# Kernel tuning notes

Measured on AMD Instinct MI355X. Metric: run time of the kernel, lower is better.

## Reference

```python
import jax, jax.numpy as jnp
import numpy as np

GROUP = 128  # WNA16 quantization group size along input dim


def dequant_uint4(packed, scale, zp):
    """packed: [..., K//2] int32 holding two uint4 nibbles per element.
    scale, zp: [..., K//GROUP] float. Returns [..., K] float weights."""
    lo = jnp.bitwise_and(packed, 15)
    hi = jnp.bitwise_and(jnp.right_shift(packed, 4), 15)
    q = jnp.stack([lo, hi], axis=-1).reshape(*packed.shape[:-1], -1)  # [..., K]
    K = q.shape[-1]
    qg = q.astype(scale.dtype).reshape(*q.shape[:-1], K // GROUP, GROUP)
    w = (qg - zp[..., None]) * scale[..., None]
    return w.reshape(*q.shape)


def setup_inputs() -> dict:
    key = jax.random.key(0)
    ks = jax.random.split(key, 9)
    E, T, D, I = 8, 2048, 2048, 2816
    s13 = 1.0 / (8.0 * np.sqrt(D))   # keep dequantized weights ~unit-variance scale
    s2 = 1.0 / (8.0 * np.sqrt(I))
    x = jax.random.normal(ks[0], (T, D), jnp.float32)
    topk_ids = jax.random.randint(ks[1], (T, 2), 0, E, dtype=jnp.int32)
    tw = jax.random.uniform(ks[2], (T, 2), jnp.float32) + 0.1
    topk_weights = tw / tw.sum(-1, keepdims=True)
    w13_packed = jax.random.randint(ks[3], (E, 2 * I, D // 2), 0, 256, dtype=jnp.int32)
    w13_scale = (jax.random.uniform(ks[4], (E, 2 * I, D // GROUP), jnp.float32) + 0.5) * s13
    w13_zp = jax.random.uniform(ks[5], (E, 2 * I, D // GROUP), jnp.float32) * 16.0
    w2_packed = jax.random.randint(ks[6], (E, D, I // 2), 0, 256, dtype=jnp.int32)
    w2_scale = (jax.random.uniform(ks[7], (E, D, I // GROUP), jnp.float32) + 0.5) * s2
    w2_zp = jax.random.uniform(ks[8], (E, D, I // GROUP), jnp.float32) * 16.0
    return {"x": x, "topk_ids": topk_ids, "topk_weights": topk_weights,
            "w13_packed": w13_packed, "w13_scale": w13_scale, "w13_zp": w13_zp,
            "w2_packed": w2_packed, "w2_scale": w2_scale, "w2_zp": w2_zp}


def reference(x, topk_ids, topk_weights, w13_packed, w13_scale, w13_zp,
              w2_packed, w2_scale, w2_zp):
    E = w13_packed.shape[0]
    # Dequantize per-expert int4 weights (the get_dequant_weight loop)
    W13 = dequant_uint4(w13_packed, w13_scale, w13_zp)   # [E, 2I, D]
    W2 = dequant_uint4(w2_packed, w2_scale, w2_zp)       # [E, D, I]
    # mixture_of_experts with silu activation: gate/up proj, silu-mul, down proj
    gate_up = jnp.einsum('td,eid->tei', x, W13)           # [T, E, 2I]
    g, u = jnp.split(gate_up, 2, axis=-1)
    h = jax.nn.silu(g) * u                                # [T, E, I]
    y = jnp.einsum('tei,edi->ted', h, W2)                 # [T, E, D]
    # combine top-k routed experts with router weights
    route = jnp.einsum('tke,tk->te',
                       jax.nn.one_hot(topk_ids, E, dtype=x.dtype), topk_weights)
    out = jnp.einsum('ted,te->td', y, route)              # [T, D]
    return out
```

## Files before the change

### kernel.cpp

```cpp
#include <hip/hip_runtime.h>
#include <hip/hip_bf16.h>

#define T_TOK 2048
#define DDIM  2048
#define IDIM  2816
#define NE    8
#define NPAIR (T_TOK*2)
#define GU_N  (2*IDIM)

typedef __bf16  bf16x8 __attribute__((ext_vector_type(8)));
typedef float   f32x4  __attribute__((ext_vector_type(4)));
typedef int     int4v  __attribute__((ext_vector_type(4)));
typedef unsigned int uint4v __attribute__((ext_vector_type(4)));

#define OFF_A   (64*1024)
#define OFF_GU  (OFF_A  + (size_t)NPAIR*DDIM*2)
#define OFF_H   (OFF_GU + (size_t)NPAIR*GU_N*2)
#define OFF_YP  (OFF_H  + (size_t)NPAIR*IDIM*2)
#define W13_DWORDS (NE*(size_t)GU_N*(DDIM/8))
#define W2_DWORDS  (NE*(size_t)DDIM*(IDIM/8))

__device__ __forceinline__ unsigned short f2bf(float f) {
    __hip_bfloat16 h = __float2bfloat16(f);
    return __builtin_bit_cast(unsigned short, h);
}
__device__ __forceinline__ float bf2f(unsigned short u) {
    unsigned int x = ((unsigned int)u) << 16;
    return __builtin_bit_cast(float, x);
}
__device__ __forceinline__ unsigned int pack2bf(float lo, float hi) {
    return ((unsigned int)f2bf(hi) << 16) | (unsigned int)f2bf(lo);
}
__device__ __forceinline__ void gload_lds16(const void* g, void* l) {
    __builtin_amdgcn_global_load_lds(
        (const __attribute__((address_space(1))) void*)g,
        (__attribute__((address_space(3))) void*)l, 16, 0, 0);
}

__global__ void route_kernel(const int* __restrict__ ids, int* __restrict__ meta) {
    __shared__ int histL[NE][256];
    __shared__ int totals[NE];
    __shared__ int offsS[NE];
    const int tid = threadIdx.x;
    for (int e = 0; e < NE; ++e) histL[e][tid] = 0;
    for (int j = 0; j < 16; ++j) {
        int id = ids[tid*16 + j];
        histL[id][tid]++;
    }
    __syncthreads();
    if (tid < NE) {
        int run = 0;
        for (int i = 0; i < 256; ++i) { int v = histL[tid][i]; histL[tid][i] = run; run += v; }
        totals[tid] = run;
    }
    __syncthreads();
    if (tid == 0) {
        int run = 0;
        for (int e = 0; e < NE; ++e) {
            offsS[e] = run;
            meta[e] = totals[e];
            meta[8+e] = run;
            run += totals[e];
        }
    }
    __syncthreads();
    for (int j = 0; j < 16; ++j) {
        int p = tid*16 + j;
        int id = ids[p];
        int local = histL[id][tid];
        histL[id][tid] = local + 1;
        meta[64 + offsS[id] + local] = p;
    }
}

__global__ void gather_kernel(const float* __restrict__ x, const int* __restrict__ meta,
                              unsigned short* __restrict__ Aall) {
    const int r = blockIdx.x;
    const int p = meta[64 + r];
    const int t = p >> 1;
    const int c = threadIdx.x * 8;
    const float4* src = (const float4*)(x + (size_t)t*DDIM + c);
    float4 f0 = src[0], f1 = src[1];
    unsigned short o[8];
    o[0]=f2bf(f0.x); o[1]=f2bf(f0.y); o[2]=f2bf(f0.z); o[3]=f2bf(f0.w);
    o[4]=f2bf(f1.x); o[5]=f2bf(f1.y); o[6]=f2bf(f1.z); o[7]=f2bf(f1.w);
    int cb  = c * 2;
    int cbs = (cb & ~127) | ((cb & 127) ^ ((r & 7) << 4));
    *(uint4v*)((char*)Aall + (size_t)r*(DDIM*2) + cbs) = *(uint4v*)o;
}

__global__ void repack_kernel(const int* __restrict__ src,
                              unsigned int* __restrict__ dst, int nwords4) {
    const int i4 = blockIdx.x * 256 + threadIdx.x;
    if (i4 >= nwords4) return;
    const int4v* s = (const int4v*)(src + (size_t)i4*16);
    uint4v d;
#pragma unroll
    for (int q = 0; q < 4; ++q) {
        int4v p = s[q];
        d[q] = ((unsigned int)p[0] & 0xFFu)
             | (((unsigned int)p[1] & 0xFFu) << 8)
             | (((unsigned int)p[2] & 0xFFu) << 16)
             | (((unsigned int)p[3] & 0xFFu) << 24);
    }
    *(uint4v*)(dst + (size_t)i4*4) = d;
}

#define LOADB(PK, SS, ZZ, KT)  do {                                        \
    PK = *(const uint4v*)(bgp + (size_t)(KT)*8);                           \
    int _g = (KT) >> 1;                                                    \
    SS = sp[_g]; ZZ = zp[_g];                                              \
} while (0)

#define ISSUE_A(SEL, KT) do {                                              \
    _Pragma("unroll")                                                      \
    for (int _i = 0; _i < 4; ++_i)                                         \
        gload_lds16(a_src[_i] + (size_t)(KT)*128,                          \
                    (char*)&As[SEL][0] + wv*4096 + _i*1024 + lane*16);     \
} while (0)

#define DEQ(PK, SS, ZZ, BWP) do {                                          \
    float _s = SS, _c = -(ZZ)*(SS);                                        \
    _Pragma("unroll")                                                      \
    for (int _q = 0; _q < 4; ++_q) {                                       \
        unsigned int _w  = PK[_q];                                         \
        unsigned int _lo = _w & 0x0F0F0F0Fu;                               \
        unsigned int _hi = (_w >> 4) & 0x0F0F0F0Fu;                        \
        _Pragma("unroll")                                                  \
        for (int _j = 0; _j < 4; ++_j) {                                   \
            float _flo = (float)((_lo >> (8*_j)) & 0xFFu);                 \
            float _fhi = (float)((_hi >> (8*_j)) & 0xFFu);                 \
            BWP[_q*4 + _j] = pack2bf(fmaf(_flo, _s, _c),                   \
                                     fmaf(_fhi, _s, _c));                  \
        }                                                                  \
    }                                                                      \
} while (0)

#define WRITE_BS(BWP) do {                                                 \
    _Pragma("unroll")                                                      \
    for (int _q = 0; _q < 4; ++_q) {                                       \
        int _cb  = ahalf*64 + _q*16;                                       \
        int _cbs = _cb ^ swzB;                                             \
        *(uint4v*)(&Bs[arow*64 + (_cbs >> 1)]) = *(uint4v*)(&BWP[_q*4]);   \
    }                                                                      \
} while (0)

#define MFMA_STEP(SEL) do {                                                \
    _Pragma("unroll")                                                      \
    for (int _kk = 0; _kk < 2; ++_kk) {                                    \
        bf16x8 _af[4], _bf[4];                                             \
        const int _kbyte = _kk*64 + lk*16;                                 \
        _Pragma("unroll")                                                  \
        for (int _mi = 0; _mi < 4; ++_mi) {                                \
            int _row = wm + _mi*16 + lr;                                   \
            int _b = _kbyte ^ (((_row + base7) & 7) << 4);                 \
            _af[_mi] = *(const bf16x8*)(&As[SEL][_row*64 + (_b >> 1)]);    \
        }                                                                  \
        _Pragma("unroll")                                                  \
        for (int _nj = 0; _nj < 4; ++_nj) {                                \
            int _row = wn + _nj*16 + lr;                                   \
            int _b = _kbyte ^ ((_row & 7) << 4);                           \
            _bf[_nj] = *(const bf16x8*)(&Bs[_row*64 + (_b >> 1)]);         \
        }                                                                  \
        _Pragma("unroll")                                                  \
        for (int _mi = 0; _mi < 4; ++_mi)                                  \
            _Pragma("unroll")                                              \
            for (int _nj = 0; _nj < 4; ++_nj)                              \
                acc[_mi][_nj] = __builtin_amdgcn_mfma_f32_16x16x32_bf16(   \
                    _af[_mi], _bf[_nj], acc[_mi][_nj], 0, 0, 0);           \
    }                                                                      \
} while (0)

#define STEP(T, SELC, SELN, PKC, sC, zC, PKN, sN, zN) do {                 \
    if ((T) > 0) __syncthreads();                                          \
    int _ktn = (T)+1 < NT ? (T)+1 : NT-1;                                  \
    ISSUE_A(SELN, _ktn);                                                   \
    LOADB(PKN, sN, zN, _ktn);                                              \
    unsigned int _bw[16];                                                  \
    DEQ(PKC, sC, zC, _bw);                                                 \
    WRITE_BS(_bw);                                                         \
    __syncthreads();                                                       \
    MFMA_STEP(SELC);                                                       \
} while (0)

__launch_bounds__(256, 3)
__global__ void gemm1_kernel(const unsigned short* __restrict__ Aall,
                             const unsigned int* __restrict__ wd,
                             const float* __restrict__ wsc,
                             const float* __restrict__ wzp,
                             const int* __restrict__ meta,
                             unsigned short* __restrict__ gu) {
    const int e   = blockIdx.z;
    const int cnt = meta[e];
    const int m0  = blockIdx.y * 128;
    if (m0 >= cnt) return;
    const int off = meta[8 + e];
    const int n0  = blockIdx.x * 128;
    const int tid = threadIdx.x;

    __shared__ unsigned short As[2][128*64];
    __shared__ unsigned short Bs[128*64];

    f32x4 acc[4][4];
#pragma unroll
    for (int i = 0; i < 4; ++i)
#pragma unroll
        for (int j = 0; j < 4; ++j) acc[i][j] = (f32x4)0.0f;

    const int arow  = tid >> 1;
    const int ahalf = tid & 1;
    const int gbrow = n0 + arow;
    const unsigned int* bgp = wd + ((size_t)e*GU_N + gbrow)*(DDIM/8) + ahalf*4;
    const float* sp = wsc + ((size_t)e*GU_N + gbrow)*(DDIM/128);
    const float* zp = wzp + ((size_t)e*GU_N + gbrow)*(DDIM/128);
    const int swzB  = (arow & 7) << 4;

    const int lane = tid & 63;
    const int wv   = tid >> 6;
    const char* a_src[4];
#pragma unroll
    for (int i = 0; i < 4; ++i) {
        int lrow  = wv*32 + i*8 + (lane >> 3);
        int garow = off + m0 + lrow; if (garow > NPAIR-1) garow = NPAIR-1;
        a_src[i] = (const char*)Aall + (size_t)garow*(DDIM*2) + (lane & 7)*16;
    }
    const int base7 = (off + m0) & 7;

    const int wm = (wv >> 1) * 64, wn = (wv & 1) * 64;
    const int lr = lane & 15, lk = lane >> 4;

    const int NT = DDIM/64;
    uint4v pkX, pkY;
    float sX, zX, sY, zY;

    ISSUE_A(0, 0);
    LOADB(pkX, sX, zX, 0);
    for (int kt = 0; kt < NT; kt += 2) {
        STEP(kt,   0, 1, pkX, sX, zX, pkY, sY, zY);
        STEP(kt+1, 1, 0, pkY, sY, zY, pkX, sX, zX);
    }

#pragma unroll
    for (int mi = 0; mi < 4; ++mi)
#pragma unroll
        for (int nj = 0; nj < 4; ++nj) {
            f32x4 v = acc[mi][nj];
            int col = n0 + wn + nj*16 + lr;
#pragma unroll
            for (int r = 0; r < 4; ++r) {
                int row = wm + mi*16 + lk*4 + r;
                if (m0 + row < cnt)
                    gu[(size_t)(off + m0 + row)*GU_N + col] = f2bf(v[r]);
            }
        }
}

__global__ void act_kernel(const unsigned short* __restrict__ gu,
                           unsigned short* __restrict__ h) {
    const int r = blockIdx.x;
    for (int c = threadIdx.x; c < IDIM/8; c += 256) {
        uint4v g8 = *(const uint4v*)(&gu[(size_t)r*GU_N + c*8]);
        uint4v u8 = *(const uint4v*)(&gu[(size_t)r*GU_N + IDIM + c*8]);
        const unsigned short* gp = (const unsigned short*)&g8;
        const unsigned short* up = (const unsigned short*)&u8;
        unsigned short o[8];
#pragma unroll
        for (int j = 0; j < 8; ++j) {
            float g = bf2f(gp[j]), u = bf2f(up[j]);
            float sg = g / (1.0f + __expf(-g));
            o[j] = f2bf(sg * u);
        }
        int cb  = c * 16;
        int cbs = (cb & ~127) | ((cb & 127) ^ ((r & 7) << 4));
        *(uint4v*)((char*)h + (size_t)r*(IDIM*2) + cbs) = *(uint4v*)o;
    }
}

__launch_bounds__(256, 3)
__global__ void gemm2_kernel(const unsigned short* __restrict__ h,
                             const unsigned int* __restrict__ wd,
                             const float* __restrict__ wsc,
                             const float* __restrict__ wzp,
                             const float* __restrict__ tw,
                             const int* __restrict__ meta,
                             float* __restrict__ yp) {
    const int e   = blockIdx.z;
    const int cnt = meta[e];
    const int m0  = blockIdx.y * 128;
    if (m0 >= cnt) return;
    const int off = meta[8 + e];
    const int n0  = blockIdx.x * 128;
    const int tid = threadIdx.x;

    __shared__ unsigned short As[2][128*64];
    __shared__ unsigned short Bs[128*64];

    f32x4 acc[4][4];
#pragma unroll
    for (int i = 0; i < 4; ++i)
#pragma unroll
        for (int j = 0; j < 4; ++j) acc[i][j] = (f32x4)0.0f;

    const int arow  = tid >> 1;
    const int ahalf = tid & 1;
    const int gbrow = n0 + arow;
    const unsigned int* bgp = wd + ((size_t)e*DDIM + gbrow)*(IDIM/8) + ahalf*4;
    const float* sp = wsc + ((size_t)e*DDIM + gbrow)*(IDIM/128);
    const float* zp = wzp + ((size_t)e*DDIM + gbrow)*(IDIM/128);
    const int swzB  = (arow & 7) << 4;

    const int lane = tid & 63;
    const int wv   = tid >> 6;
    const char* a_src[4];
#pragma unroll
    for (int i = 0; i < 4; ++i) {
        int lrow  = wv*32 + i*8 + (lane >> 3);
        int garow = off + m0 + lrow; if (garow > NPAIR-1) garow = NPAIR-1;
        a_src[i] = (const char*)h + (size_t)garow*(IDIM*2) + (lane & 7)*16;
    }
    const int base7 = (off + m0) & 7;

    const int wm = (wv >> 1) * 64, wn = (wv & 1) * 64;
    const int lr = lane & 15, lk = lane >> 4;

    const int NT = IDIM/64;
    uint4v pkX, pkY;
    float sX, zX, sY, zY;

    ISSUE_A(0, 0);
    LOADB(pkX, sX, zX, 0);
    for (int kt = 0; kt < NT; kt += 2) {
        STEP(kt,   0, 1, pkX, sX, zX, pkY, sY, zY);
        STEP(kt+1, 1, 0, pkY, sY, zY, pkX, sX, zX);
    }

#pragma unroll
    for (int mi = 0; mi < 4; ++mi)
#pragma unroll
        for (int nj = 0; nj < 4; ++nj) {
            f32x4 v = acc[mi][nj];
            int col = n0 + wn + nj*16 + lr;
#pragma unroll
            for (int r = 0; r < 4; ++r) {
                int row = wm + mi*16 + lk*4 + r;
                if (m0 + row < cnt) {
                    int p = meta[64 + off + m0 + row];
                    float w = tw[p];
                    yp[(size_t)p*DDIM + col] = v[r] * w;
                }
            }
        }
}

__global__ void combine_kernel(const float* __restrict__ yp, float* __restrict__ out) {
    const int i = blockIdx.x * 256 + threadIdx.x;
    const int t = i >> 9, d = i & 511;
    const f32x4* a = (const f32x4*)yp;
    f32x4 va = a[(size_t)(t*2)*512 + d];
    f32x4 vb = a[(size_t)(t*2+1)*512 + d];
    ((f32x4*)out)[i] = va + vb;
}

extern "C" void kernel_launch(void* const* d_in, const int* in_sizes, int n_in,
                              void* d_out, int out_size, void* d_ws, size_t ws_size,
                              hipStream_t stream) {
    const float* x    = (const float*)d_in[0];
    const int*   ids  = (const int*)d_in[1];
    const float* tw   = (const float*)d_in[2];
    const int*   w13p = (const int*)d_in[3];
    const float* w13s = (const float*)d_in[4];
    const float* w13z = (const float*)d_in[5];
    const int*   w2p  = (const int*)d_in[6];
    const float* w2s  = (const float*)d_in[7];
    const float* w2z  = (const float*)d_in[8];
    float* out = (float*)d_out;

    char* ws = (char*)d_ws;
    int* meta = (int*)ws;
    unsigned short* Aall = (unsigned short*)(ws + OFF_A);
    unsigned short* gu   = (unsigned short*)(ws + OFF_GU);
    unsigned short* h    = (unsigned short*)(ws + OFF_H);
    float* yp            = (float*)(ws + OFF_YP);
    unsigned int* W13d = (unsigned int*)(ws + OFF_H);
    unsigned int* W2d  = (unsigned int*)(ws + OFF_GU);

    route_kernel<<<1, 256, 0, stream>>>(ids, meta);
    gather_kernel<<<NPAIR, 256, 0, stream>>>(x, meta, Aall);
    repack_kernel<<<(int)(W13_DWORDS/1024), 256, 0, stream>>>(w13p, W13d, (int)(W13_DWORDS/4));
    gemm1_kernel<<<dim3(GU_N/128, NPAIR/128, NE), 256, 0, stream>>>(Aall, W13d, w13s, w13z, meta, gu);
    act_kernel<<<NPAIR, 256, 0, stream>>>(gu, h);
    repack_kernel<<<(int)(W2_DWORDS/1024), 256, 0, stream>>>(w2p, W2d, (int)(W2_DWORDS/4));
    gemm2_kernel<<<dim3(DDIM/128, NPAIR/128, NE), 256, 0, stream>>>(h, W2d, w2s, w2z, tw, meta, yp);
    combine_kernel<<<(T_TOK*DDIM/4)/256, 256, 0, stream>>>(yp, out);
}
```

Baseline: 376.1 us.

## Fuse SiLU-mul into gemm1 epilogue, atomic combine in gemm2, XCD-aware block remap

Gemm1 now computes matching gate and up columns in the same tile, interleaving 64 gate rows and 64 up rows of W13. It applies silu(g)*u in the epilogue through LDS and writes h directly, which removes the gu buffer round trip and the separate activation kernel. Gemm2 accumulates the weighted outputs straight into out with float atomics after a zeroing kernel, replacing the yp buffer and the combine kernel. Both GEMMs remap the block index so that blocks sharing a weight panel land on the same XCD, which should improve L2 reuse. Float atomics make the summation order nondeterministic, and the workspace layout is reshuffled to fit.

```diff
diff --git a/kernel.cpp b/kernel.cpp
--- a/kernel.cpp
+++ b/kernel.cpp
@@ -104,6 +104,11 @@
              | (((unsigned int)p[3] & 0xFFu) << 24);
     }
     *(uint4v*)(dst + (size_t)i4*4) = d;
+}
+
+__global__ void zero_kernel(float* __restrict__ out) {
+    const int i = blockIdx.x * 256 + threadIdx.x;
+    ((f32x4*)out)[i] = (f32x4)0.0f;
 }
 
 #define LOADB(PK, SS, ZZ, KT)  do {                                        \
@@ -189,13 +194,17 @@
                              const float* __restrict__ wsc,
                              const float* __restrict__ wzp,
                              const int* __restrict__ meta,
-                             unsigned short* __restrict__ gu) {
-    const int e   = blockIdx.z;
+                             unsigned short* __restrict__ h) {
+    const unsigned int l = blockIdx.x + 44u*(blockIdx.y + 32u*blockIdx.z);
+    const int xcd   = l & 7;
+    const int j     = l >> 3;
+    const int panel = xcd + 8*(j >> 5);
+    const int e   = panel / 44;
+    const int nx  = panel % 44;
+    const int m0  = (j & 31) * 128;
     const int cnt = meta[e];
-    const int m0  = blockIdx.y * 128;
     if (m0 >= cnt) return;
     const int off = meta[8 + e];
-    const int n0  = blockIdx.x * 128;
     const int tid = threadIdx.x;
 
     __shared__ unsigned short As[2][128*64];
@@ -205,14 +214,14 @@
 #pragma unroll
     for (int i = 0; i < 4; ++i)
 #pragma unroll
-        for (int j = 0; j < 4; ++j) acc[i][j] = (f32x4)0.0f;
+        for (int jj = 0; jj < 4; ++jj) acc[i][jj] = (f32x4)0.0f;
 
     const int arow  = tid >> 1;
     const int ahalf = tid & 1;
-    const int gbrow = n0 + arow;
-    const unsigned int* bgp = wd + ((size_t)e*GU_N + gbrow)*(DDIM/8) + ahalf*4;
-    const float* sp = wsc + ((size_t)e*GU_N + gbrow)*(DDIM/128);
-    const float* zp = wzp + ((size_t)e*GU_N + gbrow)*(DDIM/128);
+    const int brow_g = (arow < 64) ? (nx*64 + arow) : (IDIM + nx*64 + (arow - 64));
+    const unsigned int* bgp = wd + ((size_t)e*GU_N + brow_g)*(DDIM/8) + ahalf*4;
+    const float* sp = wsc + ((size_t)e*GU_N + brow_g)*(DDIM/128);
+    const float* zp = wzp + ((size_t)e*GU_N + brow_g)*(DDIM/128);
     const int swzB  = (arow & 7) << 4;
 
     const int lane = tid & 63;
@@ -239,40 +248,52 @@
         STEP(kt,   0, 1, pkX, sX, zX, pkY, sY, zY);
         STEP(kt+1, 1, 0, pkY, sY, zY, pkX, sX, zX);
     }
-
-#pragma unroll
-    for (int mi = 0; mi < 4; ++mi)
-#pragma unroll
-        for (int nj = 0; nj < 4; ++nj) {
-            f32x4 v = acc[mi][nj];
-            int col = n0 + wn + nj*16 + lr;
-#pragma unroll
-            for (int r = 0; r < 4; ++r) {
-                int row = wm + mi*16 + lk*4 + r;
-                if (m0 + row < cnt)
-                    gu[(size_t)(off + m0 + row)*GU_N + col] = f2bf(v[r]);
+    __syncthreads();
+
+    float* uf = (float*)&As[0][0];
+    if (wn == 64) {
+#pragma unroll
+        for (int mi = 0; mi < 4; ++mi)
+#pragma unroll
+            for (int nj = 0; nj < 4; ++nj) {
+                f32x4 v = acc[mi][nj];
+                int c = nj*16 + lr;
+#pragma unroll
+                for (int r = 0; r < 4; ++r)
+                    uf[(wm + mi*16 + lk*4 + r)*64 + c] = v[r];
             }
+    }
+    __syncthreads();
+    unsigned short* hb = (unsigned short*)Bs;
+    if (wn == 0) {
+#pragma unroll
+        for (int mi = 0; mi < 4; ++mi)
+#pragma unroll
+            for (int nj = 0; nj < 4; ++nj) {
+                f32x4 v = acc[mi][nj];
+                int c = nj*16 + lr;
+#pragma unroll
+                for (int r = 0; r < 4; ++r) {
+                    int row = wm + mi*16 + lk*4 + r;
+                    float g = v[r];
+                    float u = uf[row*64 + c];
+                    float sg = g / (1.0f + __expf(-g));
+                    hb[row*64 + c] = f2bf(sg * u);
+                }
+            }
+    }
+    __syncthreads();
+#pragma unroll
+    for (int q = 0; q < 4; ++q) {
+        int ci  = tid + 256*q;
+        int row = ci >> 3;
+        int k16 = ci & 7;
+        if (m0 + row < cnt) {
+            int grow = off + m0 + row;
+            int cbs  = (k16*16) ^ ((grow & 7) << 4);
+            *(uint4v*)((char*)h + (size_t)grow*(IDIM*2) + nx*128 + cbs) =
+                *(uint4v*)&hb[row*64 + k16*8];
         }
-}
-
-__global__ void act_kernel(const unsigned short* __restrict__ gu,
-                           unsigned short* __restrict__ h) {
-    const int r = blockIdx.x;
-    for (int c = threadIdx.x; c < IDIM/8; c += 256) {
-        uint4v g8 = *(const uint4v*)(&gu[(size_t)r*GU_N + c*8]);
-        uint4v u8 = *(const uint4v*)(&gu[(size_t)r*GU_N + IDIM + c*8]);
-        const unsigned short* gp = (const unsigned short*)&g8;
-        const unsigned short* up = (const unsigned short*)&u8;
-        unsigned short o[8];
-#pragma unroll
-        for (int j = 0; j < 8; ++j) {
-            float g = bf2f(gp[j]), u = bf2f(up[j]);
-            float sg = g / (1.0f + __expf(-g));
-            o[j] = f2bf(sg * u);
-        }
-        int cb  = c * 16;
-        int cbs = (cb & ~127) | ((cb & 127) ^ ((r & 7) << 4));
-        *(uint4v*)((char*)h + (size_t)r*(IDIM*2) + cbs) = *(uint4v*)o;
     }
 }
 
@@ -283,13 +304,17 @@
                              const float* __restrict__ wzp,
                              const float* __restrict__ tw,
                              const int* __restrict__ meta,
-                             float* __restrict__ yp) {
-    const int e   = blockIdx.z;
+                             float* __restrict__ out) {
+    const unsigned int l = blockIdx.x + 16u*(blockIdx.y + 32u*blockIdx.z);
+    const int xcd   = l & 7;
+    const int j     = l >> 3;
+    const int panel = xcd + 8*(j >> 5);
+    const int e   = panel / 16;
+    const int n0  = (panel % 16) * 128;
+    const int m0  = (j & 31) * 128;
     const int cnt = meta[e];
-    const int m0  = blockIdx.y * 128;
     if (m0 >= cnt) return;
     const int off = meta[8 + e];
-    const int n0  = blockIdx.x * 128;
     const int tid = threadIdx.x;
 
     __shared__ unsigned short As[2][128*64];
@@ -299,7 +324,7 @@
 #pragma unroll
     for (int i = 0; i < 4; ++i)
 #pragma unroll
-        for (int j = 0; j < 4; ++j) acc[i][j] = (f32x4)0.0f;
+        for (int jj = 0; jj < 4; ++jj) acc[i][jj] = (f32x4)0.0f;
 
     const int arow  = tid >> 1;
     const int ahalf = tid & 1;
@@ -333,6 +358,7 @@
         STEP(kt,   0, 1, pkX, sX, zX, pkY, sY, zY);
         STEP(kt+1, 1, 0, pkY, sY, zY, pkX, sX, zX);
     }
+    __syncthreads();
 
 #pragma unroll
     for (int mi = 0; mi < 4; ++mi)
@@ -346,19 +372,10 @@
                 if (m0 + row < cnt) {
                     int p = meta[64 + off + m0 + row];
                     float w = tw[p];
-                    yp[(size_t)p*DDIM + col] = v[r] * w;
+                    unsafeAtomicAdd(&out[(size_t)(p >> 1)*DDIM + col], v[r] * w);
                 }
             }
         }
-}
-
-__global__ void combine_kernel(const float* __restrict__ yp, float* __restrict__ out) {
-    const int i = blockIdx.x * 256 + threadIdx.x;
-    const int t = i >> 9, d = i & 511;
-    const f32x4* a = (const f32x4*)yp;
-    f32x4 va = a[(size_t)(t*2)*512 + d];
-    f32x4 vb = a[(size_t)(t*2+1)*512 + d];
-    ((f32x4*)out)[i] = va + vb;
 }
 
 extern "C" void kernel_launch(void* const* d_in, const int* in_sizes, int n_in,
@@ -378,18 +395,15 @@
     char* ws = (char*)d_ws;
     int* meta = (int*)ws;
     unsigned short* Aall = (unsigned short*)(ws + OFF_A);
-    unsigned short* gu   = (unsigned short*)(ws + OFF_GU);
     unsigned short* h    = (unsigned short*)(ws + OFF_H);
-    float* yp            = (float*)(ws + OFF_YP);
-    unsigned int* W13d = (unsigned int*)(ws + OFF_H);
-    unsigned int* W2d  = (unsigned int*)(ws + OFF_GU);
+    unsigned int* W13d   = (unsigned int*)(ws + OFF_GU);
+    unsigned int* W2d    = (unsigned int*)(ws + OFF_YP);
 
     route_kernel<<<1, 256, 0, stream>>>(ids, meta);
     gather_kernel<<<NPAIR, 256, 0, stream>>>(x, meta, Aall);
     repack_kernel<<<(int)(W13_DWORDS/1024), 256, 0, stream>>>(w13p, W13d, (int)(W13_DWORDS/4));
-    gemm1_kernel<<<dim3(GU_N/128, NPAIR/128, NE), 256, 0, stream>>>(Aall, W13d, w13s, w13z, meta, gu);
-    act_kernel<<<NPAIR, 256, 0, stream>>>(gu, h);
+    gemm1_kernel<<<dim3(44, NPAIR/128, NE), 256, 0, stream>>>(Aall, W13d, w13s, w13z, meta, h);
     repack_kernel<<<(int)(W2_DWORDS/1024), 256, 0, stream>>>(w2p, W2d, (int)(W2_DWORDS/4));
-    gemm2_kernel<<<dim3(DDIM/128, NPAIR/128, NE), 256, 0, stream>>>(h, W2d, w2s, w2z, tw, meta, yp);
-    combine_kernel<<<(T_TOK*DDIM/4)/256, 256, 0, stream>>>(yp, out);
-}
+    zero_kernel<<<(T_TOK*DDIM/4)/256, 256, 0, stream>>>(out);
+    gemm2_kernel<<<dim3(DDIM/128, NPAIR/128, NE), 256, 0, stream>>>(h, W2d, w2s, w2z, tw, meta, out);
+}
```

After: 483.5 us. +28.5%, slower.

## Fuse SiLU-gate activation into gemm1 epilogue by interleaving gate/up rows per tile

Applied to the files above, without the earlier changes.

Each gemm1 block now loads 64 gate rows and their 64 matching up rows, interleaved in 16-column groups, so the epilogue holds both gate and up accumulators and writes silu(g)*u straight into the swizzled h buffer. This drops the separate activation kernel and the round trip of the 2I-wide gate/up intermediate through global memory. The trade-off is scattered 2-byte stores in the epilogue instead of 16-byte vector stores, and a reshuffled workspace layout.

```diff
diff --git a/kernel.cpp b/kernel.cpp
--- a/kernel.cpp
+++ b/kernel.cpp
@@ -189,13 +189,13 @@
                              const float* __restrict__ wsc,
                              const float* __restrict__ wzp,
                              const int* __restrict__ meta,
-                             unsigned short* __restrict__ gu) {
+                             unsigned short* __restrict__ h) {
     const int e   = blockIdx.z;
     const int cnt = meta[e];
     const int m0  = blockIdx.y * 128;
     if (m0 >= cnt) return;
     const int off = meta[8 + e];
-    const int n0  = blockIdx.x * 128;
+    const int n0h = blockIdx.x * 64;
     const int tid = threadIdx.x;
 
     __shared__ unsigned short As[2][128*64];
@@ -209,7 +209,9 @@
 
     const int arow  = tid >> 1;
     const int ahalf = tid & 1;
-    const int gbrow = n0 + arow;
+    const int hcl   = ((arow >> 5) << 4) + (arow & 15);
+    const int is_up = (arow >> 4) & 1;
+    const int gbrow = is_up ? (IDIM + n0h + hcl) : (n0h + hcl);
     const unsigned int* bgp = wd + ((size_t)e*GU_N + gbrow)*(DDIM/8) + ahalf*4;
     const float* sp = wsc + ((size_t)e*GU_N + gbrow)*(DDIM/128);
     const float* zp = wzp + ((size_t)e*GU_N + gbrow)*(DDIM/128);
@@ -243,37 +245,24 @@
 #pragma unroll
     for (int mi = 0; mi < 4; ++mi)
 #pragma unroll
-        for (int nj = 0; nj < 4; ++nj) {
-            f32x4 v = acc[mi][nj];
-            int col = n0 + wn + nj*16 + lr;
+        for (int cp = 0; cp < 2; ++cp) {
+            f32x4 g = acc[mi][cp*2];
+            f32x4 u = acc[mi][cp*2 + 1];
+            int col = n0h + ((wn >> 5) + cp)*16 + lr;
+            int cb  = col * 2;
 #pragma unroll
             for (int r = 0; r < 4; ++r) {
                 int row = wm + mi*16 + lk*4 + r;
-                if (m0 + row < cnt)
-                    gu[(size_t)(off + m0 + row)*GU_N + col] = f2bf(v[r]);
+                if (m0 + row < cnt) {
+                    int grow = off + m0 + row;
+                    float gg = g[r];
+                    float sg = gg / (1.0f + __expf(-gg));
+                    int cbs = (cb & ~127) | ((cb & 127) ^ ((grow & 7) << 4));
+                    *(unsigned short*)((char*)h + (size_t)grow*(IDIM*2) + cbs)
+                        = f2bf(sg * u[r]);
+                }
             }
         }
-}
-
-__global__ void act_kernel(const unsigned short* __restrict__ gu,
-                           unsigned short* __restrict__ h) {
-    const int r = blockIdx.x;
-    for (int c = threadIdx.x; c < IDIM/8; c += 256) {
-        uint4v g8 = *(const uint4v*)(&gu[(size_t)r*GU_N + c*8]);
-        uint4v u8 = *(const uint4v*)(&gu[(size_t)r*GU_N + IDIM + c*8]);
-        const unsigned short* gp = (const unsigned short*)&g8;
-        const unsigned short* up = (const unsigned short*)&u8;
-        unsigned short o[8];
-#pragma unroll
-        for (int j = 0; j < 8; ++j) {
-            float g = bf2f(gp[j]), u = bf2f(up[j]);
-            float sg = g / (1.0f + __expf(-g));
-            o[j] = f2bf(sg * u);
-        }
-        int cb  = c * 16;
-        int cbs = (cb & ~127) | ((cb & 127) ^ ((r & 7) << 4));
-        *(uint4v*)((char*)h + (size_t)r*(IDIM*2) + cbs) = *(uint4v*)o;
-    }
 }
 
 __launch_bounds__(256, 3)
@@ -378,17 +367,15 @@
     char* ws = (char*)d_ws;
     int* meta = (int*)ws;
     unsigned short* Aall = (unsigned short*)(ws + OFF_A);
-    unsigned short* gu   = (unsigned short*)(ws + OFF_GU);
     unsigned short* h    = (unsigned short*)(ws + OFF_H);
     float* yp            = (float*)(ws + OFF_YP);
-    unsigned int* W13d = (unsigned int*)(ws + OFF_H);
+    unsigned int* W13d = (unsigned int*)(ws + OFF_GU);
     unsigned int* W2d  = (unsigned int*)(ws + OFF_GU);
 
     route_kernel<<<1, 256, 0, stream>>>(ids, meta);
     gather_kernel<<<NPAIR, 256, 0, stream>>>(x, meta, Aall);
     repack_kernel<<<(int)(W13_DWORDS/1024), 256, 0, stream>>>(w13p, W13d, (int)(W13_DWORDS/4));
-    gemm1_kernel<<<dim3(GU_N/128, NPAIR/128, NE), 256, 0, stream>>>(Aall, W13d, w13s, w13z, meta, gu);
-    act_kernel<<<NPAIR, 256, 0, stream>>>(gu, h);
+    gemm1_kernel<<<dim3(IDIM/64, NPAIR/128, NE), 256, 0, stream>>>(Aall, W13d, w13s, w13z, meta, h);
     repack_kernel<<<(int)(W2_DWORDS/1024), 256, 0, stream>>>(w2p, W2d, (int)(W2_DWORDS/4));
     gemm2_kernel<<<dim3(DDIM/128, NPAIR/128, NE), 256, 0, stream>>>(h, W2d, w2s, w2z, tw, meta, yp);
     combine_kernel<<<(T_TOK*DDIM/4)/256, 256, 0, stream>>>(yp, out);
```

New measurement: 366.2 us, median of 3. 1.03x faster.
